# Optimization experiments

Hardware: AMD Instinct MI355X
Metric: run time of the kernel (lower is better)

The kernel has to match this reference:

```python
import jax, jax.numpy as jnp
import numpy as np

T, N, E = 12, 50000, 1_600_000
IN_DIM, H, H2, H3, AF, B = 12, 128, 256, 128, 10, 4096


def _sage(h, src, dst, Wl, Wr, b, n_nodes):
    # PyG SAGEConv (mean aggr): out = lin_l(mean_{j in N(i)} x_j) + lin_r(x_i)
    agg = jax.ops.segment_sum(h[src], dst, num_segments=n_nodes)
    deg = jax.ops.segment_sum(jnp.ones((src.shape[0],), h.dtype), dst, num_segments=n_nodes)
    mean = agg / jnp.clip(deg, 1.0)[:, None]
    return mean @ Wl.T + b + h @ Wr.T


def _attn(h, Wq, bq, Wk, bk, Wv, bv):
    # h: [N, T, H]; queries scaled by 1/sqrt(H) AFTER the linear (as in source)
    q = (h @ Wq.T + bq) / jnp.sqrt(jnp.asarray(h.shape[-1], h.dtype))
    k = h @ Wk.T + bk
    v = h @ Wv.T + bv
    w = jax.nn.softmax(jnp.einsum('nth,nsh->nts', q, k), axis=-1)
    return jnp.einsum('nts,nsh->nth', w, v)


def setup_inputs() -> dict:
    key = jax.random.key(0)
    ks = jax.random.split(key, 24)
    def lin(kw, out_d, in_d, scale=None):
        s = scale if scale is not None else 1.0 / np.sqrt(in_d)
        return jax.random.uniform(kw, (out_d, in_d), jnp.float32, -s, s)
    inp = {
        'x': jax.random.normal(ks[0], (T, N, IN_DIM), jnp.float32),
        'edge_index': jax.random.randint(ks[1], (2, E), 0, N, jnp.int64),
        'node_idx': jax.random.randint(ks[2], (B,), 0, N, jnp.int64),
        'apart_feature': jax.random.normal(ks[3], (B, AF), jnp.float32),
        'conv1_Wl': lin(ks[4], H, IN_DIM), 'conv1_Wr': lin(ks[5], H, IN_DIM),
        'conv1_b': jnp.zeros((H,), jnp.float32),
        'conv2_Wl': lin(ks[6], H, H), 'conv2_Wr': lin(ks[7], H, H),
        'conv2_b': jnp.zeros((H,), jnp.float32),
        'Wq': lin(ks[8], H, H), 'bq': jnp.zeros((H,), jnp.float32),
        'Wk': lin(ks[9], H, H), 'bk': jnp.zeros((H,), jnp.float32),
        'Wv': lin(ks[10], H, H), 'bv': jnp.zeros((H,), jnp.float32),
        'fc1_W': lin(ks[11], H2, H + AF), 'fc1_b': jnp.zeros((H2,), jnp.float32),
        'fc2_W': lin(ks[12], H3, H2), 'fc2_b': jnp.zeros((H3,), jnp.float32),
        'fc3_W': lin(ks[13], 1, H3), 'fc3_b': jnp.zeros((1,), jnp.float32),
    }
    return inp


def reference(x, edge_index, node_idx, apart_feature,
              conv1_Wl, conv1_Wr, conv1_b, conv2_Wl, conv2_Wr, conv2_b,
              Wq, bq, Wk, bk, Wv, bv,
              fc1_W, fc1_b, fc2_W, fc2_b, fc3_W, fc3_b):
    src, dst = edge_index[0], edge_index[1]
    n_nodes = x.shape[1]
    # conv1 per time slot (small fixed loop over T, matching the source)
    emb = jnp.stack([
        jax.nn.relu(_sage(x[i], src, dst, conv1_Wl, conv1_Wr, conv1_b, n_nodes))
        for i in range(x.shape[0])], axis=0)  # [T, N, H]
    emb = _attn(emb.transpose(1, 0, 2), Wq, bq, Wk, bk, Wv, bv).transpose(1, 0, 2)  # [T, N, H]
    emb = jnp.stack([
        jax.nn.relu(_sage(emb[i], src, dst, conv2_Wl, conv2_Wr, conv2_b, n_nodes))
        for i in range(emb.shape[0])], axis=0)  # [T, N, H]
    emb = _attn(emb.transpose(1, 0, 2), Wq, bq, Wk, bk, Wv, bv).sum(axis=1)  # [N, H]
    h = jnp.concatenate([emb[node_idx], apart_feature], axis=1)  # [B, H+AF]
    h = jax.nn.leaky_relu(h @ fc1_W.T + fc1_b, negative_slope=0.1)
    h = jax.nn.leaky_relu(h @ fc2_W.T + fc2_b, negative_slope=0.05)
    return h @ fc3_W.T + fc3_b  # [B, 1]
```

## Files before the change

### kernel.cpp

```cpp
#include <hip/hip_runtime.h>
#include <hip/hip_bf16.h>
#include <cstddef>
#include <cstdint>
#include <cmath>

typedef __attribute__((ext_vector_type(8))) short bf16x8v;
typedef __attribute__((ext_vector_type(4))) float f32x4;

__device__ inline unsigned short f2bf(float x) {
    uint32_t u = __float_as_uint(x);
    uint32_t r = (u + 0x7fffu + ((u >> 16) & 1u)) >> 16;
    return (unsigned short)r;
}

__device__ inline uint32_t pack2(float a, float b) {
    return (uint32_t)f2bf(a) | ((uint32_t)f2bf(b) << 16);
}

__device__ inline void unpack8(bf16x8v v, float* f) {
    union { bf16x8v v8; uint32_t u[4]; } cv; cv.v8 = v;
    #pragma unroll
    for (int d = 0; d < 4; d++) {
        uint32_t w = cv.u[d];
        f[2 * d]     = __uint_as_float(w << 16);
        f[2 * d + 1] = __uint_as_float(w & 0xffff0000u);
    }
}


__global__ __launch_bounds__(256) void prep0_kernel(
    const float* __restrict__ x, unsigned short* __restrict__ xTb, int N, int TB,
    const float* __restrict__ c2Wl, const float* __restrict__ c2Wr,
    const float* __restrict__ fc1W, const float* __restrict__ fc2W,
    const float* __restrict__ Wq, const float* __restrict__ Wk, const float* __restrict__ Wv,
    const float* __restrict__ c1Wl, const float* __restrict__ c1Wr,
    const float* __restrict__ bq,
    unsigned short* __restrict__ W2pack,
    float* __restrict__ fc1Wt, float* __restrict__ fc2Wt,
    unsigned short* __restrict__ Bpack, unsigned short* __restrict__ W1pack,
    unsigned short* __restrict__ Mpack, float* __restrict__ rvec,
    int* __restrict__ deg, int* __restrict__ cur) {
    __shared__ __align__(16) unsigned short sm[64][144];
    int b = blockIdx.x;
    int tid = threadIdx.x;
    if (b < TB) {
        int n0 = b * 64;
        int nodes = min(64, N - n0);
        for (int t = 0; t < 12; t++) {
            const float* src = x + ((size_t)t * N + n0) * 12;
            for (int k = tid; k < nodes * 12; k += 256)
                sm[k / 12][t * 12 + k % 12] = f2bf(src[k]);
        }
        __syncthreads();
        int chunks = nodes * 18;
        const uint4* smv = (const uint4*)&sm[0][0];
        uint4* dst = (uint4*)(xTb + (size_t)n0 * 144);
        for (int c = tid; c < chunks; c += 256) dst[c] = smv[c];
        return;
    }
    b -= TB;
    if (b < 667) {
        const float qscale = 0.08838834764831845f;
        int idx = b * 256 + tid;
        if (idx < 32768) {
            int i = idx & 7, l = (idx >> 3) & 63, nt = (idx >> 9) & 7, kc = idx >> 12;
            int col = nt * 16 + (l & 15);
            int k = kc * 32 + (l >> 4) * 8 + i;
            float v = (k < 128) ? c2Wl[col * 128 + k] : c2Wr[col * 128 + k - 128];
            W2pack[idx] = f2bf(v);
            return;
        }
        idx -= 32768;
        if (idx < 35328) { fc1Wt[(idx % 138) * 256 + idx / 138] = fc1W[idx]; return; }
        idx -= 35328;
        if (idx < 32768) { fc2Wt[(idx % 256) * 128 + idx / 256] = fc2W[idx]; return; }
        idx -= 32768;
        if (idx < 3 * 16384) {
            int p = idx >> 14, rem = idx & 16383;
            int kc = rem >> 12, rem2 = rem & 4095;
            int nt = rem2 >> 9, li = rem2 & 511;
            int l = li >> 3, i = li & 7;
            int col = nt * 16 + (l & 15);
            int j = kc * 32 + (l >> 4) * 8 + i;
            const float* W = (p == 0) ? Wq : (p == 1) ? Wk : Wv;
            Bpack[idx] = f2bf(W[col * 128 + j]);
            return;
        }
        idx -= 3 * 16384;
        if (idx < 4096) {
            int nt = idx >> 9, rem = idx & 511;
            int l = rem >> 3, i = rem & 7;
            int col = nt * 16 + (l & 15);
            int k = (l >> 4) * 8 + i;
            float v = (k < 12) ? c1Wl[col * 12 + k] : ((k < 24) ? c1Wr[col * 12 + k - 12] : 0.0f);
            W1pack[idx] = f2bf(v);
            return;
        }
        idx -= 4096;
        if (idx < 16384) {
            int kc = idx >> 12, rem2 = idx & 4095;
            int nt = rem2 >> 9, li = rem2 & 511;
            int l = li >> 3, i = li & 7;
            int col = nt * 16 + (l & 15);
            int j = kc * 32 + (l >> 4) * 8 + i;
            float sum = 0.f;
            for (int c = 0; c < 128; c++) sum += Wq[c * 128 + j] * Wk[c * 128 + col];
            Mpack[idx] = f2bf(qscale * sum);
            return;
        }
        idx -= 16384;
        if (idx < 128) {
            float sum = 0.f;
            for (int c = 0; c < 128; c++) sum += bq[c] * Wk[c * 128 + idx];
            rvec[idx] = qscale * sum;
        }
        return;
    }
    b -= 667;
    int idx = b * 256 + tid;
    if (idx < N) deg[idx] = 0;
    else if (idx < 2 * N) cur[idx - N] = 0;
}

__global__ void deg_kernel(const int* __restrict__ ei, int* __restrict__ deg, int E) {
    int e = blockIdx.x * 256 + threadIdx.x;
    if (e < E) atomicAdd(&deg[ei[E + e]], 1);
}

__global__ void scan_kernel(const int* __restrict__ deg, int* __restrict__ rs, int N) {
    __shared__ int part[1024];
    int tid = threadIdx.x;
    int chunk = (N + 1023) >> 10;
    int base = tid * chunk;
    int s = 0;
    for (int k = 0; k < chunk; k++) { int i = base + k; if (i < N) s += deg[i]; }
    part[tid] = s;
    __syncthreads();
    for (int off = 1; off < 1024; off <<= 1) {
        int v = (tid >= off) ? part[tid - off] : 0;
        __syncthreads();
        part[tid] += v;
        __syncthreads();
    }
    int run = part[tid] - s;
    for (int k = 0; k < chunk; k++) {
        int i = base + k;
        if (i < N) { rs[i] = run; run += deg[i]; }
    }
    if (tid == 1023) rs[N] = part[1023];
}

__global__ void fill_kernel(const int* __restrict__ ei, const int* __restrict__ rs,
                            int* __restrict__ cur, int* __restrict__ csr, int E) {
    int e = blockIdx.x * 256 + threadIdx.x;
    if (e < E) {
        int d = ei[E + e];
        int pos = atomicAdd(&cur[d], 1);
        csr[rs[d] + pos] = ei[e];
    }
}

__global__ void sentinel_kernel(float* out, int n) {
    int i = blockIdx.x * 256 + threadIdx.x;
    if (i < n) out[i] = 12345.0f;
}


__global__ __launch_bounds__(128) void fused1_kernel(
    const unsigned short* __restrict__ xTb, const int* __restrict__ rs,
    const int* __restrict__ csr, const unsigned short* __restrict__ W1pack,
    const float* __restrict__ b1, const unsigned short* __restrict__ Mpack,
    const float* __restrict__ rvec, const unsigned short* __restrict__ Vpack,
    const float* __restrict__ bv, unsigned short* __restrict__ emb1, int N) {
    __shared__ __align__(16) unsigned short lds[8448];
    int tid = threadIdx.x;
    int w = tid >> 6, l = tid & 63;
    int g = l >> 4, lam = l & 15;
    int node = blockIdx.x * 2 + w;
    if (node >= N) return;
    unsigned short* L = lds + w * 4224;
    unsigned short* s_cat = L;
    float* s_part = (float*)(L + 2176);
    const bf16x8v zero8 = (bf16x8v){0, 0, 0, 0, 0, 0, 0, 0};

    int beg = rs[node], end = rs[node + 1];
    int group = l / 18, d8 = l - group * 18;
    if (group < 3) {
        float acc[8] = {0.f, 0.f, 0.f, 0.f, 0.f, 0.f, 0.f, 0.f};
        int e = beg + group;
        for (; e + 21 < end; e += 24) {
            int nn[8];
            #pragma unroll
            for (int u = 0; u < 8; u++) nn[u] = csr[e + u * 3];
            bf16x8v vv[8];
            #pragma unroll
            for (int u = 0; u < 8; u++)
                vv[u] = *(const bf16x8v*)(xTb + (size_t)nn[u] * 144 + d8 * 8);
            #pragma unroll
            for (int u = 0; u < 8; u++) {
                float f[8]; unpack8(vv[u], f);
                #pragma unroll
                for (int i = 0; i < 8; i++) acc[i] += f[i];
            }
        }
        for (; e + 9 < end; e += 12) {
            int n0 = csr[e], n1 = csr[e + 3], n2 = csr[e + 6], n3 = csr[e + 9];
            bf16x8v v0 = *(const bf16x8v*)(xTb + (size_t)n0 * 144 + d8 * 8);
            bf16x8v v1 = *(const bf16x8v*)(xTb + (size_t)n1 * 144 + d8 * 8);
            bf16x8v v2 = *(const bf16x8v*)(xTb + (size_t)n2 * 144 + d8 * 8);
            bf16x8v v3 = *(const bf16x8v*)(xTb + (size_t)n3 * 144 + d8 * 8);
            float f0[8], f1[8], f2[8], f3[8];
            unpack8(v0, f0); unpack8(v1, f1); unpack8(v2, f2); unpack8(v3, f3);
            #pragma unroll
            for (int i = 0; i < 8; i++) acc[i] += (f0[i] + f1[i]) + (f2[i] + f3[i]);
        }
        for (; e < end; e += 3) {
            int nbr = csr[e];
            bf16x8v v = *(const bf16x8v*)(xTb + (size_t)nbr * 144 + d8 * 8);
            float f[8]; unpack8(v, f);
            #pragma unroll
            for (int i = 0; i < 8; i++) acc[i] += f[i];
        }
        #pragma unroll
        for (int i = 0; i < 8; i++) s_part[group * 144 + i * 18 + d8] = acc[i];
    }
    if (l < 16) *(uint4*)&s_cat[l * 40 + 24] = make_uint4(0u, 0u, 0u, 0u);
    if (l < 18) {
        float inv = 1.0f / fmaxf((float)(end - beg), 1.0f);
        bf16x8v sv = *(const bf16x8v*)(xTb + (size_t)node * 144 + l * 8);
        #pragma unroll
        for (int i = 0; i < 8; i++) {
            int d = l * 8 + i;
            int t = d / 12, f = d - t * 12;
            int j = i * 18 + l;
            float m = (s_part[j] + s_part[144 + j] + s_part[288 + j]) * inv;
            s_cat[t * 40 + f] = f2bf(m);
            s_cat[t * 40 + 12 + f] = ((unsigned short*)&sv)[i];
        }
    }

    bf16x8v a1 = (lam < 12) ? *(const bf16x8v*)&s_cat[lam * 40 + g * 8] : zero8;
    bf16x8v bfa[8];
    #pragma unroll
    for (int nt = 0; nt < 8; nt++) bfa[nt] = *(const bf16x8v*)(W1pack + nt * 512 + l * 8);
    f32x4 c1[8];
    #pragma unroll
    for (int nt = 0; nt < 8; nt++)
        c1[nt] = __builtin_amdgcn_mfma_f32_16x16x32_bf16(a1, bfa[nt], (f32x4){0.f, 0.f, 0.f, 0.f}, 0, 0, 0);
    #pragma unroll
    for (int nt = 0; nt < 8; nt++) {
        float bias = b1[nt * 16 + lam];
        #pragma unroll
        for (int r = 0; r < 4; r++)
            L[(4 * g + r) * 136 + nt * 16 + lam] = f2bf(fmaxf(c1[nt][r] + bias, 0.0f));
    }

    bf16x8v ha[4];
    #pragma unroll
    for (int kc = 0; kc < 4; kc++)
        ha[kc] = (lam < 12) ? *(const bf16x8v*)&L[lam * 136 + kc * 32 + g * 8] : zero8;

    f32x4 cg[8];
    #pragma unroll
    for (int nt = 0; nt < 8; nt++) cg[nt] = (f32x4){0.f, 0.f, 0.f, 0.f};
    #pragma unroll
    for (int kc = 0; kc < 4; kc++) {
        #pragma unroll
        for (int nt = 0; nt < 8; nt++)
            bfa[nt] = *(const bf16x8v*)(Mpack + (kc * 8 + nt) * 512 + l * 8);
        #pragma unroll
        for (int nt = 0; nt < 8; nt++)
            cg[nt] = __builtin_amdgcn_mfma_f32_16x16x32_bf16(ha[kc], bfa[nt], cg[nt], 0, 0, 0);
    }
    #pragma unroll
    for (int nt = 0; nt < 8; nt++) {
        float rv = rvec[nt * 16 + lam];
        #pragma unroll
        for (int r = 0; r < 4; r++)
            L[(4 * g + r) * 136 + nt * 16 + lam] = f2bf(cg[nt][r] + rv);
    }

    f32x4 cv[8];
    #pragma unroll
    for (int nt = 0; nt < 8; nt++) cv[nt] = (f32x4){0.f, 0.f, 0.f, 0.f};
    #pragma unroll
    for (int kc = 0; kc < 4; kc++) {
        #pragma unroll
        for (int nt = 0; nt < 8; nt++)
            bfa[nt] = *(const bf16x8v*)(Vpack + (kc * 8 + nt) * 512 + l * 8);
        #pragma unroll
        for (int nt = 0; nt < 8; nt++)
            cv[nt] = __builtin_amdgcn_mfma_f32_16x16x32_bf16(ha[kc], bfa[nt], cv[nt], 0, 0, 0);
    }
    #pragma unroll
    for (int nt = 0; nt < 8; nt++) {
        float bb = bv[nt * 16 + lam];
        uint32_t w0 = pack2(cv[nt][0] + bb, cv[nt][1] + bb);
        uint32_t w1 = pack2(cv[nt][2] + bb, cv[nt][3] + bb);
        *(uint2*)&L[2176 + (nt * 16 + lam) * 16 + 4 * g] = make_uint2(w0, w1);
    }

    f32x4 sc = (f32x4){0.f, 0.f, 0.f, 0.f};
    #pragma unroll
    for (int kc = 0; kc < 4; kc++) {
        bf16x8v ga = (lam < 12) ? *(const bf16x8v*)&L[lam * 136 + kc * 32 + g * 8] : zero8;
        sc = __builtin_amdgcn_mfma_f32_16x16x32_bf16(ga, ha[kc], sc, 0, 0, 0);
    }
    #pragma unroll
    for (int r = 0; r < 4; r++) {
        float s = (lam < 12) ? sc[r] : -3.0e38f;
        float mx = s;
        mx = fmaxf(mx, __shfl_xor(mx, 1)); mx = fmaxf(mx, __shfl_xor(mx, 2));
        mx = fmaxf(mx, __shfl_xor(mx, 4)); mx = fmaxf(mx, __shfl_xor(mx, 8));
        float e = __expf(s - mx);
        float sm = e;
        sm += __shfl_xor(sm, 1); sm += __shfl_xor(sm, 2);
        sm += __shfl_xor(sm, 4); sm += __shfl_xor(sm, 8);
        L[(4 * g + r) * 16 + lam] = f2bf(e / sm);
    }

    bf16x8v bw = (g < 2) ? *(const bf16x8v*)&L[lam * 16 + g * 8] : zero8;
    #pragma unroll
    for (int nt = 0; nt < 8; nt++) {
        bf16x8v av = (g < 2) ? *(const bf16x8v*)&L[2176 + (nt * 16 + lam) * 16 + g * 8] : zero8;
        f32x4 o = __builtin_amdgcn_mfma_f32_16x16x32_bf16(av, bw, (f32x4){0.f, 0.f, 0.f, 0.f}, 0, 0, 0);
        if (lam < 12) {
            uint32_t w0 = pack2(o[0], o[1]);
            uint32_t w1 = pack2(o[2], o[3]);
            *(uint2*)(emb1 + (size_t)node * 1536 + lam * 128 + nt * 16 + 4 * g) = make_uint2(w0, w1);
        }
    }
}


template <int SUM>
__global__ __launch_bounds__(64) void mfma_attn_kernel(
    unsigned short* io, const unsigned short* __restrict__ Bpack,
    const float* __restrict__ bq, const float* __restrict__ bk, const float* __restrict__ bv,
    float* __restrict__ outF, int totalRows) {
    __shared__ __align__(16) unsigned short lds[19712];
    int l = threadIdx.x;
    int g = l >> 4, lam = l & 15;
    int baseRow = blockIdx.x * 48;

    bf16x8v afrag[3][4];
    #pragma unroll
    for (int rt = 0; rt < 3; rt++) {
        int row = baseRow + rt * 16 + lam;
        if (row > totalRows - 1) row = totalRows - 1;
        #pragma unroll
        for (int kc = 0; kc < 4; kc++)
            afrag[rt][kc] = *(const bf16x8v*)(io + (size_t)row * 128 + kc * 32 + g * 8);
    }
    const float qscale = 0.08838834764831845f;

    #pragma unroll
    for (int p = 0; p < 3; p++) {
        f32x4 acc[3][8];
        #pragma unroll
        for (int rt = 0; rt < 3; rt++)
            #pragma unroll
            for (int nt = 0; nt < 8; nt++) acc[rt][nt] = (f32x4){0.f, 0.f, 0.f, 0.f};
        const unsigned short* Bp = Bpack + p * 16384;
        #pragma unroll
        for (int kc = 0; kc < 4; kc++) {
            #pragma unroll
            for (int nt = 0; nt < 8; nt++) {
                bf16x8v bfrag = *(const bf16x8v*)(Bp + (kc * 8 + nt) * 512 + l * 8);
                #pragma unroll
                for (int rt = 0; rt < 3; rt++)
                    acc[rt][nt] = __builtin_amdgcn_mfma_f32_16x16x32_bf16(afrag[rt][kc], bfrag, acc[rt][nt], 0, 0, 0);
            }
        }
        const float* bias = (p == 0) ? bq : (p == 1) ? bk : bv;
        #pragma unroll
        for (int nt = 0; nt < 8; nt++) {
            float bval = bias[nt * 16 + lam];
            #pragma unroll
            for (int rt = 0; rt < 3; rt++) {
                int row0 = 16 * rt + 4 * g;
                if (p < 2) {
                    int base = (p == 0) ? 0 : 6528;
                    #pragma unroll
                    for (int r = 0; r < 4; r++) {
                        float val = acc[rt][nt][r] + bval;
                        if (p == 0) val *= qscale;
                        lds[base + (row0 + r) * 136 + nt * 16 + lam] = f2bf(val);
                    }
                } else {
                    uint32_t w0 = pack2(acc[rt][nt][0] + bval, acc[rt][nt][1] + bval);
                    uint32_t w1 = pack2(acc[rt][nt][2] + bval, acc[rt][nt][3] + bval);
                    *(uint2*)&lds[13056 + (nt * 16 + lam) * 52 + row0] = make_uint2(w0, w1);
                }
            }
        }
    }
    __syncthreads();

    float wv[4][4];
    #pragma unroll
    for (int n = 0; n < 4; n++) {
        int qrow = 12 * n + lam;
        if (qrow > 47) qrow = 47;
        f32x4 sc = (f32x4){0.f, 0.f, 0.f, 0.f};
        #pragma unroll
        for (int kc = 0; kc < 4; kc++) {
            bf16x8v qa = *(const bf16x8v*)&lds[qrow * 136 + kc * 32 + g * 8];
            bf16x8v kb = *(const bf16x8v*)&lds[6528 + qrow * 136 + kc * 32 + g * 8];
            sc = __builtin_amdgcn_mfma_f32_16x16x32_bf16(qa, kb, sc, 0, 0, 0);
        }
        #pragma unroll
        for (int r = 0; r < 4; r++) {
            float s = (lam < 12) ? sc[r] : -3.0e38f;
            float mx = s;
            mx = fmaxf(mx, __shfl_xor(mx, 1)); mx = fmaxf(mx, __shfl_xor(mx, 2));
            mx = fmaxf(mx, __shfl_xor(mx, 4)); mx = fmaxf(mx, __shfl_xor(mx, 8));
            float e = __expf(s - mx);
            float sm = e;
            sm += __shfl_xor(sm, 1); sm += __shfl_xor(sm, 2);
            sm += __shfl_xor(sm, 4); sm += __shfl_xor(sm, 8);
            wv[n][r] = e / sm;
        }
    }
    __syncthreads();
    #pragma unroll
    for (int n = 0; n < 4; n++)
        #pragma unroll
        for (int r = 0; r < 4; r++)
            lds[(n * 16 + 4 * g + r) * 24 + lam] = f2bf(wv[n][r]);
    __syncthreads();

    const bf16x8v zero8 = (bf16x8v){0, 0, 0, 0, 0, 0, 0, 0};
    #pragma unroll
    for (int n = 0; n < 4; n++) {
        bf16x8v wfrag = zero8;
        if (g < 2) wfrag = *(const bf16x8v*)&lds[(n * 16 + lam) * 24 + g * 8];
        int sA = 12 * n + g * 8;
        int sB = sA + 4;
        if (sB > 44) sB = 44;
        #pragma unroll
        for (int nt = 0; nt < 8; nt++) {
            bf16x8v vfrag = zero8;
            if (g < 2) {
                int dbase = 13056 + (nt * 16 + lam) * 52;
                uint2 lo = *(const uint2*)&lds[dbase + sA];
                uint2 hi = *(const uint2*)&lds[dbase + sB];
                union { uint32_t u[4]; bf16x8v v; } cvv;
                cvv.u[0] = lo.x; cvv.u[1] = lo.y; cvv.u[2] = hi.x; cvv.u[3] = hi.y;
                vfrag = cvv.v;
            }
            f32x4 o = __builtin_amdgcn_mfma_f32_16x16x32_bf16(vfrag, wfrag, (f32x4){0.f, 0.f, 0.f, 0.f}, 0, 0, 0);
            if constexpr (SUM == 0) {
                if (lam < 12) {
                    int row = baseRow + 12 * n + lam;
                    if (row < totalRows) {
                        uint32_t w0 = pack2(o[0], o[1]);
                        uint32_t w1 = pack2(o[2], o[3]);
                        *(uint2*)(io + (size_t)row * 128 + nt * 16 + 4 * g) = make_uint2(w0, w1);
                    }
                }
            } else {
                #pragma unroll
                for (int r = 0; r < 4; r++) {
                    float v = (lam < 12) ? o[r] : 0.f;
                    v += __shfl_xor(v, 1); v += __shfl_xor(v, 2);
                    v += __shfl_xor(v, 4); v += __shfl_xor(v, 8);
                    o[r] = v;
                }
                if (lam == 0 && (baseRow + 12 * n) < totalRows) {
                    int node = blockIdx.x * 4 + n;
                    *(float4*)(outF + (size_t)node * 128 + nt * 16 + 4 * g) =
                        make_float4(o[0], o[1], o[2], o[3]);
                }
            }
        }
    }
}


__global__ __launch_bounds__(256) void conv2_kernel(
    const unsigned short* __restrict__ emb1, const int* __restrict__ node_idx,
    const int* __restrict__ rs, const int* __restrict__ csr,
    const unsigned short* __restrict__ W2pack, const float* __restrict__ b2,
    unsigned short* __restrict__ emb2) {
    int bb = blockIdx.x, tid = threadIdx.x;
    int n = node_idx[bb];
    __shared__ __align__(16) unsigned short s_cat[12][264];
    __shared__ __align__(16) unsigned short s_tile[12][128];
    int beg = rs[n], end = rs[n + 1];
    if (tid < 192) {
        float acc[8] = {0.f, 0.f, 0.f, 0.f, 0.f, 0.f, 0.f, 0.f};
        int e = beg;
        for (; e + 3 < end; e += 4) {
            int n0 = csr[e], n1 = csr[e + 1], n2 = csr[e + 2], n3 = csr[e + 3];
            bf16x8v v0 = *(const bf16x8v*)(emb1 + (size_t)n0 * 1536 + tid * 8);
            bf16x8v v1 = *(const bf16x8v*)(emb1 + (size_t)n1 * 1536 + tid * 8);
            bf16x8v v2 = *(const bf16x8v*)(emb1 + (size_t)n2 * 1536 + tid * 8);
            bf16x8v v3 = *(const bf16x8v*)(emb1 + (size_t)n3 * 1536 + tid * 8);
            float f0[8], f1[8], f2[8], f3[8];
            unpack8(v0, f0); unpack8(v1, f1); unpack8(v2, f2); unpack8(v3, f3);
            #pragma unroll
            for (int i = 0; i < 8; i++) acc[i] += (f0[i] + f1[i]) + (f2[i] + f3[i]);
        }
        for (; e < end; e++) {
            int nbr = csr[e];
            bf16x8v v = *(const bf16x8v*)(emb1 + (size_t)nbr * 1536 + tid * 8);
            float f[8]; unpack8(v, f);
            #pragma unroll
            for (int i = 0; i < 8; i++) acc[i] += f[i];
        }
        float inv = 1.0f / fmaxf((float)(end - beg), 1.0f);
        uint32_t w[4];
        #pragma unroll
        for (int d = 0; d < 4; d++)
            w[d] = pack2(acc[2 * d] * inv, acc[2 * d + 1] * inv);
        *(uint4*)&s_cat[tid >> 4][(tid & 15) * 8] = make_uint4(w[0], w[1], w[2], w[3]);
    } else {
        for (int c = tid - 192; c < 192; c += 64) {
            uint4 v = *(const uint4*)(emb1 + (size_t)n * 1536 + c * 8);
            *(uint4*)&s_cat[c >> 4][128 + (c & 15) * 8] = v;
        }
    }
    __syncthreads();
    if (tid < 64) {
        int g = tid >> 4, lam = tid & 15;
        const bf16x8v zero8 = (bf16x8v){0, 0, 0, 0, 0, 0, 0, 0};
        f32x4 acc2[8];
        #pragma unroll
        for (int nt = 0; nt < 8; nt++) acc2[nt] = (f32x4){0.f, 0.f, 0.f, 0.f};
        #pragma unroll
        for (int kc = 0; kc < 8; kc++) {
            bf16x8v a = (lam < 12) ? *(const bf16x8v*)&s_cat[lam][kc * 32 + g * 8] : zero8;
            #pragma unroll
            for (int nt = 0; nt < 8; nt++) {
                bf16x8v bf = *(const bf16x8v*)(W2pack + (kc * 8 + nt) * 512 + tid * 8);
                acc2[nt] = __builtin_amdgcn_mfma_f32_16x16x32_bf16(a, bf, acc2[nt], 0, 0, 0);
            }
        }
        if (g < 3) {
            #pragma unroll
            for (int nt = 0; nt < 8; nt++) {
                float bias = b2[nt * 16 + lam];
                #pragma unroll
                for (int r = 0; r < 4; r++)
                    s_tile[4 * g + r][nt * 16 + lam] = f2bf(fmaxf(acc2[nt][r] + bias, 0.0f));
            }
        }
    }
    __syncthreads();
    if (tid < 192)
        ((uint4*)(emb2 + (size_t)bb * 1536))[tid] = ((const uint4*)&s_tile[0][0])[tid];
}


__global__ __launch_bounds__(256) void head_kernel(
    const float* __restrict__ embF, const float* __restrict__ apart, const float* __restrict__ fc1Wt,
    const float* __restrict__ fc1b, const float* __restrict__ fc2Wt, const float* __restrict__ fc2b,
    const float* __restrict__ fc3W, const float* __restrict__ fc3b, float* __restrict__ out) {
    int bb = blockIdx.x, tid = threadIdx.x;
    __shared__ float in_s[138], a1[256], a2[128], red[128];
    if (tid < 128) in_s[tid] = embF[(size_t)bb * 128 + tid];
    else if (tid < 138) in_s[tid] = apart[(size_t)bb * 10 + tid - 128];
    __syncthreads();
    float o = fc1b[tid];
    for (int j = 0; j < 138; j++) o += in_s[j] * fc1Wt[j * 256 + tid];
    a1[tid] = o >= 0.f ? o : 0.1f * o;
    __syncthreads();
    if (tid < 128) {
        float o2 = fc2b[tid];
        for (int j = 0; j < 256; j++) o2 += a1[j] * fc2Wt[j * 128 + tid];
        a2[tid] = o2 >= 0.f ? o2 : 0.05f * o2;
    }
    __syncthreads();
    if (tid < 128) red[tid] = a2[tid] * fc3W[tid];
    __syncthreads();
    for (int s = 64; s > 0; s >>= 1) {
        if (tid < s) red[tid] += red[tid + s];
        __syncthreads();
    }
    if (tid == 0) out[bb] = red[0] + fc3b[0];
}


extern "C" void kernel_launch(void* const* d_in, const int* in_sizes, int n_in,
                              void* d_out, int out_size, void* d_ws, size_t ws_size,
                              hipStream_t stream) {
    const float* x    = (const float*)d_in[0];
    const int* ei     = (const int*)d_in[1];
    const int* nidx   = (const int*)d_in[2];
    const float* apart= (const float*)d_in[3];
    const float* c1Wl = (const float*)d_in[4];
    const float* c1Wr = (const float*)d_in[5];
    const float* c1b  = (const float*)d_in[6];
    const float* c2Wl = (const float*)d_in[7];
    const float* c2Wr = (const float*)d_in[8];
    const float* c2b  = (const float*)d_in[9];
    const float* Wq   = (const float*)d_in[10];
    const float* bq   = (const float*)d_in[11];
    const float* Wk   = (const float*)d_in[12];
    const float* bk   = (const float*)d_in[13];
    const float* Wv   = (const float*)d_in[14];
    const float* bv   = (const float*)d_in[15];
    const float* fc1W = (const float*)d_in[16];
    const float* fc1b = (const float*)d_in[17];
    const float* fc2W = (const float*)d_in[18];
    const float* fc2b = (const float*)d_in[19];
    const float* fc3W = (const float*)d_in[20];
    const float* fc3b = (const float*)d_in[21];

    int N = in_sizes[0] / 144;
    int E = in_sizes[1] / 2;
    int B = in_sizes[2];
    float* out = (float*)d_out;
    char* ws = (char*)d_ws;

    size_t off = 0;
    auto A = [&](size_t bytes) -> void* {
        void* q = ws + off;
        off = (off + bytes + 255) & ~(size_t)255;
        return q;
    };
    unsigned short* emb1 = (unsigned short*)A((size_t)N * 1536 * 2);
    size_t xtBytes = (size_t)N * 144 * 2;
    unsigned short* xTb = (unsigned short*)A(xtBytes);
    unsigned short* emb2;
    if ((size_t)B * 1536 * 2 <= xtBytes) emb2 = xTb;
    else emb2 = (unsigned short*)A((size_t)B * 1536 * 2);
    float* embF  = (float*)A((size_t)B * 128 * 4);
    unsigned short* Bpack  = (unsigned short*)A(3 * 16384 * 2);
    unsigned short* W1pack = (unsigned short*)A(4096 * 2);
    unsigned short* W2pack = (unsigned short*)A(32768 * 2);
    unsigned short* Mpack  = (unsigned short*)A(16384 * 2);
    float* rvec  = (float*)A(128 * 4);
    float* fc1Wt = (float*)A(138 * 256 * 4);
    float* fc2Wt = (float*)A(256 * 128 * 4);
    int* deg = (int*)A((size_t)N * 4);
    int* rsb = (int*)A((size_t)(N + 1) * 4);
    int* cur = (int*)A((size_t)N * 4);
    int* csr = (int*)A((size_t)E * 4);
    if (off > ws_size) {
        sentinel_kernel<<<(out_size + 255) / 256, 256, 0, stream>>>(out, out_size);
        return;
    }

    int TB = (N + 63) / 64;
    int ZB = (2 * N + 255) / 256;
    prep0_kernel<<<TB + 667 + ZB, 256, 0, stream>>>(
        x, xTb, N, TB,
        c2Wl, c2Wr, fc1W, fc2W, Wq, Wk, Wv, c1Wl, c1Wr, bq,
        W2pack, fc1Wt, fc2Wt, Bpack, W1pack, Mpack, rvec, deg, cur);

    int eb = (E + 255) / 256;
    deg_kernel<<<eb, 256, 0, stream>>>(ei, deg, E);
    scan_kernel<<<1, 1024, 0, stream>>>(deg, rsb, N);
    fill_kernel<<<eb, 256, 0, stream>>>(ei, rsb, cur, csr, E);

    fused1_kernel<<<(N + 1) / 2, 128, 0, stream>>>(
        xTb, rsb, csr, W1pack, c1b, Mpack, rvec, Bpack + 2 * 16384, bv, emb1, N);

    conv2_kernel<<<B, 256, 0, stream>>>(emb1, nidx, rsb, csr, W2pack, c2b, emb2);

    int rows2 = B * 12;
    mfma_attn_kernel<1><<<(rows2 + 47) / 48, 64, 0, stream>>>(emb2, Bpack, bq, bk, bv, embF, rows2);

    head_kernel<<<B, 256, 0, stream>>>(embF, apart, fc1Wt, fc1b, fc2Wt, fc2b, fc3W, fc3b, out);
}
```

Before: 653.3 us.

## Fuse conv2, second attention and MLP head into one per-node kernel

Replaces three kernels (conv2, second attention, head) with a single kernel per batch node. The neighbour gather is unrolled by 8 instead of 4, and the attention uses the precomputed Mpack/rvec folded Q·K form already used in fused1. This removes two launches and the emb2/embF global round trips. The cost is that only one wavefront does the MFMA work while the other three sit idle, and the longer kernel holds more registers and LDS.

Measured after the change: 673.2 us. 3.0% more time.

```diff
diff --git a/kernel.cpp b/kernel.cpp
--- a/kernel.cpp
+++ b/kernel.cpp
@@ -333,81 +333,138 @@
 }
 
 
-template <int SUM>
-__global__ __launch_bounds__(64) void mfma_attn_kernel(
-    unsigned short* io, const unsigned short* __restrict__ Bpack,
-    const float* __restrict__ bq, const float* __restrict__ bk, const float* __restrict__ bv,
-    float* __restrict__ outF, int totalRows) {
-    __shared__ __align__(16) unsigned short lds[19712];
-    int l = threadIdx.x;
-    int g = l >> 4, lam = l & 15;
-    int baseRow = blockIdx.x * 48;
-
-    bf16x8v afrag[3][4];
-    #pragma unroll
-    for (int rt = 0; rt < 3; rt++) {
-        int row = baseRow + rt * 16 + lam;
-        if (row > totalRows - 1) row = totalRows - 1;
+__global__ __launch_bounds__(256) void fused2_kernel(
+    const unsigned short* __restrict__ emb1, const int* __restrict__ node_idx,
+    const int* __restrict__ rs, const int* __restrict__ csr,
+    const unsigned short* __restrict__ W2pack, const float* __restrict__ b2,
+    const unsigned short* __restrict__ Mpack, const float* __restrict__ rvec,
+    const unsigned short* __restrict__ Vpack, const float* __restrict__ bv,
+    const float* __restrict__ apart,
+    const float* __restrict__ fc1Wt, const float* __restrict__ fc1b,
+    const float* __restrict__ fc2Wt, const float* __restrict__ fc2b,
+    const float* __restrict__ fc3W, const float* __restrict__ fc3b,
+    float* __restrict__ out) {
+    __shared__ __align__(16) unsigned short s_cat[12 * 264];
+    __shared__ __align__(16) unsigned short A[4224];
+    __shared__ float hd[128];
+    __shared__ float in_s[138], ah1[256], ah2[128];
+    int bb = blockIdx.x, tid = threadIdx.x;
+    int n = node_idx[bb];
+    int beg = rs[n], end = rs[n + 1];
+    const bf16x8v zero8 = (bf16x8v){0, 0, 0, 0, 0, 0, 0, 0};
+
+    if (tid < 192) {
+        float acc[8] = {0.f, 0.f, 0.f, 0.f, 0.f, 0.f, 0.f, 0.f};
+        int e = beg;
+        for (; e + 7 < end; e += 8) {
+            int nn[8];
+            #pragma unroll
+            for (int u = 0; u < 8; u++) nn[u] = csr[e + u];
+            bf16x8v vv[8];
+            #pragma unroll
+            for (int u = 0; u < 8; u++)
+                vv[u] = *(const bf16x8v*)(emb1 + (size_t)nn[u] * 1536 + tid * 8);
+            #pragma unroll
+            for (int u = 0; u < 8; u++) {
+                float f[8]; unpack8(vv[u], f);
+                #pragma unroll
+                for (int i = 0; i < 8; i++) acc[i] += f[i];
+            }
+        }
+        for (; e < end; e++) {
+            int nbr = csr[e];
+            bf16x8v v = *(const bf16x8v*)(emb1 + (size_t)nbr * 1536 + tid * 8);
+            float f[8]; unpack8(v, f);
+            #pragma unroll
+            for (int i = 0; i < 8; i++) acc[i] += f[i];
+        }
+        float inv = 1.0f / fmaxf((float)(end - beg), 1.0f);
+        uint32_t w[4];
+        #pragma unroll
+        for (int d = 0; d < 4; d++)
+            w[d] = pack2(acc[2 * d] * inv, acc[2 * d + 1] * inv);
+        *(uint4*)&s_cat[(tid >> 4) * 264 + (tid & 15) * 8] = make_uint4(w[0], w[1], w[2], w[3]);
+    } else {
+        for (int c = tid - 192; c < 192; c += 64) {
+            uint4 v = *(const uint4*)(emb1 + (size_t)n * 1536 + c * 8);
+            *(uint4*)&s_cat[(c >> 4) * 264 + 128 + (c & 15) * 8] = v;
+        }
+    }
+    __syncthreads();
+
+    if (tid < 64) {
+        int l = tid, g = l >> 4, lam = l & 15;
+        f32x4 acc2[8];
+        #pragma unroll
+        for (int nt = 0; nt < 8; nt++) acc2[nt] = (f32x4){0.f, 0.f, 0.f, 0.f};
+        #pragma unroll
+        for (int kc = 0; kc < 8; kc++) {
+            bf16x8v a = (lam < 12) ? *(const bf16x8v*)&s_cat[lam * 264 + kc * 32 + g * 8] : zero8;
+            #pragma unroll
+            for (int nt = 0; nt < 8; nt++) {
+                bf16x8v bf = *(const bf16x8v*)(W2pack + (kc * 8 + nt) * 512 + l * 8);
+                acc2[nt] = __builtin_amdgcn_mfma_f32_16x16x32_bf16(a, bf, acc2[nt], 0, 0, 0);
+            }
+        }
+        #pragma unroll
+        for (int nt = 0; nt < 8; nt++) {
+            float bias = b2[nt * 16 + lam];
+            #pragma unroll
+            for (int r = 0; r < 4; r++)
+                A[(4 * g + r) * 136 + nt * 16 + lam] = f2bf(fmaxf(acc2[nt][r] + bias, 0.0f));
+        }
+
+        bf16x8v ha[4];
         #pragma unroll
         for (int kc = 0; kc < 4; kc++)
-            afrag[rt][kc] = *(const bf16x8v*)(io + (size_t)row * 128 + kc * 32 + g * 8);
-    }
-    const float qscale = 0.08838834764831845f;
-
-    #pragma unroll
-    for (int p = 0; p < 3; p++) {
-        f32x4 acc[3][8];
-        #pragma unroll
-        for (int rt = 0; rt < 3; rt++)
-            #pragma unroll
-            for (int nt = 0; nt < 8; nt++) acc[rt][nt] = (f32x4){0.f, 0.f, 0.f, 0.f};
-        const unsigned short* Bp = Bpack + p * 16384;
+            ha[kc] = (lam < 12) ? *(const bf16x8v*)&A[lam * 136 + kc * 32 + g * 8] : zero8;
+
+        f32x4 cg[8];
+        bf16x8v bfa[8];
+        #pragma unroll
+        for (int nt = 0; nt < 8; nt++) cg[nt] = (f32x4){0.f, 0.f, 0.f, 0.f};
         #pragma unroll
         for (int kc = 0; kc < 4; kc++) {
             #pragma unroll
-            for (int nt = 0; nt < 8; nt++) {
-                bf16x8v bfrag = *(const bf16x8v*)(Bp + (kc * 8 + nt) * 512 + l * 8);
-                #pragma unroll
-                for (int rt = 0; rt < 3; rt++)
-                    acc[rt][nt] = __builtin_amdgcn_mfma_f32_16x16x32_bf16(afrag[rt][kc], bfrag, acc[rt][nt], 0, 0, 0);
-            }
-        }
-        const float* bias = (p == 0) ? bq : (p == 1) ? bk : bv;
+            for (int nt = 0; nt < 8; nt++)
+                bfa[nt] = *(const bf16x8v*)(Mpack + (kc * 8 + nt) * 512 + l * 8);
+            #pragma unroll
+            for (int nt = 0; nt < 8; nt++)
+                cg[nt] = __builtin_amdgcn_mfma_f32_16x16x32_bf16(ha[kc], bfa[nt], cg[nt], 0, 0, 0);
+        }
         #pragma unroll
         for (int nt = 0; nt < 8; nt++) {
-            float bval = bias[nt * 16 + lam];
-            #pragma unroll
-            for (int rt = 0; rt < 3; rt++) {
-                int row0 = 16 * rt + 4 * g;
-                if (p < 2) {
-                    int base = (p == 0) ? 0 : 6528;
-                    #pragma unroll
-                    for (int r = 0; r < 4; r++) {
-                        float val = acc[rt][nt][r] + bval;
-                        if (p == 0) val *= qscale;
-                        lds[base + (row0 + r) * 136 + nt * 16 + lam] = f2bf(val);
-                    }
-                } else {
-                    uint32_t w0 = pack2(acc[rt][nt][0] + bval, acc[rt][nt][1] + bval);
-                    uint32_t w1 = pack2(acc[rt][nt][2] + bval, acc[rt][nt][3] + bval);
-                    *(uint2*)&lds[13056 + (nt * 16 + lam) * 52 + row0] = make_uint2(w0, w1);
-                }
-            }
-        }
-    }
-    __syncthreads();
-
-    float wv[4][4];
-    #pragma unroll
-    for (int n = 0; n < 4; n++) {
-        int qrow = 12 * n + lam;
-        if (qrow > 47) qrow = 47;
+            float rv = rvec[nt * 16 + lam];
+            #pragma unroll
+            for (int r = 0; r < 4; r++)
+                A[(4 * g + r) * 136 + nt * 16 + lam] = f2bf(cg[nt][r] + rv);
+        }
+
+        f32x4 cvv[8];
+        #pragma unroll
+        for (int nt = 0; nt < 8; nt++) cvv[nt] = (f32x4){0.f, 0.f, 0.f, 0.f};
+        #pragma unroll
+        for (int kc = 0; kc < 4; kc++) {
+            #pragma unroll
+            for (int nt = 0; nt < 8; nt++)
+                bfa[nt] = *(const bf16x8v*)(Vpack + (kc * 8 + nt) * 512 + l * 8);
+            #pragma unroll
+            for (int nt = 0; nt < 8; nt++)
+                cvv[nt] = __builtin_amdgcn_mfma_f32_16x16x32_bf16(ha[kc], bfa[nt], cvv[nt], 0, 0, 0);
+        }
+        #pragma unroll
+        for (int nt = 0; nt < 8; nt++) {
+            float bb2 = bv[nt * 16 + lam];
+            uint32_t w0 = pack2(cvv[nt][0] + bb2, cvv[nt][1] + bb2);
+            uint32_t w1 = pack2(cvv[nt][2] + bb2, cvv[nt][3] + bb2);
+            *(uint2*)&A[2176 + (nt * 16 + lam) * 16 + 4 * g] = make_uint2(w0, w1);
+        }
+
         f32x4 sc = (f32x4){0.f, 0.f, 0.f, 0.f};
         #pragma unroll
         for (int kc = 0; kc < 4; kc++) {
-            bf16x8v qa = *(const bf16x8v*)&lds[qrow * 136 + kc * 32 + g * 8];
-            bf16x8v kb = *(const bf16x8v*)&lds[6528 + qrow * 136 + kc * 32 + g * 8];
-            sc = __builtin_amdgcn_mfma_f32_16x16x32_bf16(qa, kb, sc, 0, 0, 0);
+            bf16x8v ga = (lam < 12) ? *(const bf16x8v*)&A[lam * 136 + kc * 32 + g * 8] : zero8;
+            sc = __builtin_amdgcn_mfma_f32_16x16x32_bf16(ga, ha[kc], sc, 0, 0, 0);
         }
         #pragma unroll
         for (int r = 0; r < 4; r++) {
@@ -419,166 +476,48 @@
             float sm = e;
             sm += __shfl_xor(sm, 1); sm += __shfl_xor(sm, 2);
             sm += __shfl_xor(sm, 4); sm += __shfl_xor(sm, 8);
-            wv[n][r] = e / sm;
+            A[(4 * g + r) * 16 + lam] = f2bf(e / sm);
+        }
+
+        bf16x8v bw = (g < 2) ? *(const bf16x8v*)&A[lam * 16 + g * 8] : zero8;
+        #pragma unroll
+        for (int nt = 0; nt < 8; nt++) {
+            bf16x8v av = (g < 2) ? *(const bf16x8v*)&A[2176 + (nt * 16 + lam) * 16 + g * 8] : zero8;
+            f32x4 o = __builtin_amdgcn_mfma_f32_16x16x32_bf16(av, bw, (f32x4){0.f, 0.f, 0.f, 0.f}, 0, 0, 0);
+            #pragma unroll
+            for (int r = 0; r < 4; r++) {
+                float v = (lam < 12) ? o[r] : 0.f;
+                v += __shfl_xor(v, 1); v += __shfl_xor(v, 2);
+                v += __shfl_xor(v, 4); v += __shfl_xor(v, 8);
+                o[r] = v;
+            }
+            if (lam == 0) {
+                #pragma unroll
+                for (int r = 0; r < 4; r++) hd[nt * 16 + 4 * g + r] = o[r];
+            }
         }
     }
     __syncthreads();
-    #pragma unroll
-    for (int n = 0; n < 4; n++)
-        #pragma unroll
-        for (int r = 0; r < 4; r++)
-            lds[(n * 16 + 4 * g + r) * 24 + lam] = f2bf(wv[n][r]);
-    __syncthreads();
-
-    const bf16x8v zero8 = (bf16x8v){0, 0, 0, 0, 0, 0, 0, 0};
-    #pragma unroll
-    for (int n = 0; n < 4; n++) {
-        bf16x8v wfrag = zero8;
-        if (g < 2) wfrag = *(const bf16x8v*)&lds[(n * 16 + lam) * 24 + g * 8];
-        int sA = 12 * n + g * 8;
-        int sB = sA + 4;
-        if (sB > 44) sB = 44;
-        #pragma unroll
-        for (int nt = 0; nt < 8; nt++) {
-            bf16x8v vfrag = zero8;
-            if (g < 2) {
-                int dbase = 13056 + (nt * 16 + lam) * 52;
-                uint2 lo = *(const uint2*)&lds[dbase + sA];
-                uint2 hi = *(const uint2*)&lds[dbase + sB];
-                union { uint32_t u[4]; bf16x8v v; } cvv;
-                cvv.u[0] = lo.x; cvv.u[1] = lo.y; cvv.u[2] = hi.x; cvv.u[3] = hi.y;
-                vfrag = cvv.v;
-            }
-            f32x4 o = __builtin_amdgcn_mfma_f32_16x16x32_bf16(vfrag, wfrag, (f32x4){0.f, 0.f, 0.f, 0.f}, 0, 0, 0);
-            if constexpr (SUM == 0) {
-                if (lam < 12) {
-                    int row = baseRow + 12 * n + lam;
-                    if (row < totalRows) {
-                        uint32_t w0 = pack2(o[0], o[1]);
-                        uint32_t w1 = pack2(o[2], o[3]);
-                        *(uint2*)(io + (size_t)row * 128 + nt * 16 + 4 * g) = make_uint2(w0, w1);
-                    }
-                }
-            } else {
-                #pragma unroll
-                for (int r = 0; r < 4; r++) {
-                    float v = (lam < 12) ? o[r] : 0.f;
-                    v += __shfl_xor(v, 1); v += __shfl_xor(v, 2);
-                    v += __shfl_xor(v, 4); v += __shfl_xor(v, 8);
-                    o[r] = v;
-                }
-                if (lam == 0 && (baseRow + 12 * n) < totalRows) {
-                    int node = blockIdx.x * 4 + n;
-                    *(float4*)(outF + (size_t)node * 128 + nt * 16 + 4 * g) =
-                        make_float4(o[0], o[1], o[2], o[3]);
-                }
-            }
-        }
-    }
-}
-
-
-__global__ __launch_bounds__(256) void conv2_kernel(
-    const unsigned short* __restrict__ emb1, const int* __restrict__ node_idx,
-    const int* __restrict__ rs, const int* __restrict__ csr,
-    const unsigned short* __restrict__ W2pack, const float* __restrict__ b2,
-    unsigned short* __restrict__ emb2) {
-    int bb = blockIdx.x, tid = threadIdx.x;
-    int n = node_idx[bb];
-    __shared__ __align__(16) unsigned short s_cat[12][264];
-    __shared__ __align__(16) unsigned short s_tile[12][128];
-    int beg = rs[n], end = rs[n + 1];
-    if (tid < 192) {
-        float acc[8] = {0.f, 0.f, 0.f, 0.f, 0.f, 0.f, 0.f, 0.f};
-        int e = beg;
-        for (; e + 3 < end; e += 4) {
-            int n0 = csr[e], n1 = csr[e + 1], n2 = csr[e + 2], n3 = csr[e + 3];
-            bf16x8v v0 = *(const bf16x8v*)(emb1 + (size_t)n0 * 1536 + tid * 8);
-            bf16x8v v1 = *(const bf16x8v*)(emb1 + (size_t)n1 * 1536 + tid * 8);
-            bf16x8v v2 = *(const bf16x8v*)(emb1 + (size_t)n2 * 1536 + tid * 8);
-            bf16x8v v3 = *(const bf16x8v*)(emb1 + (size_t)n3 * 1536 + tid * 8);
-            float f0[8], f1[8], f2[8], f3[8];
-            unpack8(v0, f0); unpack8(v1, f1); unpack8(v2, f2); unpack8(v3, f3);
-            #pragma unroll
-            for (int i = 0; i < 8; i++) acc[i] += (f0[i] + f1[i]) + (f2[i] + f3[i]);
-        }
-        for (; e < end; e++) {
-            int nbr = csr[e];
-            bf16x8v v = *(const bf16x8v*)(emb1 + (size_t)nbr * 1536 + tid * 8);
-            float f[8]; unpack8(v, f);
-            #pragma unroll
-            for (int i = 0; i < 8; i++) acc[i] += f[i];
-        }
-        float inv = 1.0f / fmaxf((float)(end - beg), 1.0f);
-        uint32_t w[4];
-        #pragma unroll
-        for (int d = 0; d < 4; d++)
-            w[d] = pack2(acc[2 * d] * inv, acc[2 * d + 1] * inv);
-        *(uint4*)&s_cat[tid >> 4][(tid & 15) * 8] = make_uint4(w[0], w[1], w[2], w[3]);
-    } else {
-        for (int c = tid - 192; c < 192; c += 64) {
-            uint4 v = *(const uint4*)(emb1 + (size_t)n * 1536 + c * 8);
-            *(uint4*)&s_cat[c >> 4][128 + (c & 15) * 8] = v;
-        }
-    }
-    __syncthreads();
-    if (tid < 64) {
-        int g = tid >> 4, lam = tid & 15;
-        const bf16x8v zero8 = (bf16x8v){0, 0, 0, 0, 0, 0, 0, 0};
-        f32x4 acc2[8];
-        #pragma unroll
-        for (int nt = 0; nt < 8; nt++) acc2[nt] = (f32x4){0.f, 0.f, 0.f, 0.f};
-        #pragma unroll
-        for (int kc = 0; kc < 8; kc++) {
-            bf16x8v a = (lam < 12) ? *(const bf16x8v*)&s_cat[lam][kc * 32 + g * 8] : zero8;
-            #pragma unroll
-            for (int nt = 0; nt < 8; nt++) {
-                bf16x8v bf = *(const bf16x8v*)(W2pack + (kc * 8 + nt) * 512 + tid * 8);
-                acc2[nt] = __builtin_amdgcn_mfma_f32_16x16x32_bf16(a, bf, acc2[nt], 0, 0, 0);
-            }
-        }
-        if (g < 3) {
-            #pragma unroll
-            for (int nt = 0; nt < 8; nt++) {
-                float bias = b2[nt * 16 + lam];
-                #pragma unroll
-                for (int r = 0; r < 4; r++)
-                    s_tile[4 * g + r][nt * 16 + lam] = f2bf(fmaxf(acc2[nt][r] + bias, 0.0f));
-            }
-        }
-    }
-    __syncthreads();
-    if (tid < 192)
-        ((uint4*)(emb2 + (size_t)bb * 1536))[tid] = ((const uint4*)&s_tile[0][0])[tid];
-}
-
-
-__global__ __launch_bounds__(256) void head_kernel(
-    const float* __restrict__ embF, const float* __restrict__ apart, const float* __restrict__ fc1Wt,
-    const float* __restrict__ fc1b, const float* __restrict__ fc2Wt, const float* __restrict__ fc2b,
-    const float* __restrict__ fc3W, const float* __restrict__ fc3b, float* __restrict__ out) {
-    int bb = blockIdx.x, tid = threadIdx.x;
-    __shared__ float in_s[138], a1[256], a2[128], red[128];
-    if (tid < 128) in_s[tid] = embF[(size_t)bb * 128 + tid];
+
+    if (tid < 128) in_s[tid] = hd[tid];
     else if (tid < 138) in_s[tid] = apart[(size_t)bb * 10 + tid - 128];
     __syncthreads();
     float o = fc1b[tid];
     for (int j = 0; j < 138; j++) o += in_s[j] * fc1Wt[j * 256 + tid];
-    a1[tid] = o >= 0.f ? o : 0.1f * o;
+    ah1[tid] = o >= 0.f ? o : 0.1f * o;
     __syncthreads();
     if (tid < 128) {
         float o2 = fc2b[tid];
-        for (int j = 0; j < 256; j++) o2 += a1[j] * fc2Wt[j * 128 + tid];
-        a2[tid] = o2 >= 0.f ? o2 : 0.05f * o2;
-    }
-    __syncthreads();
-    if (tid < 128) red[tid] = a2[tid] * fc3W[tid];
+        for (int j = 0; j < 256; j++) o2 += ah1[j] * fc2Wt[j * 128 + tid];
+        float a2 = o2 >= 0.f ? o2 : 0.05f * o2;
+        ah2[tid] = a2 * fc3W[tid];
+    }
     __syncthreads();
     for (int s = 64; s > 0; s >>= 1) {
-        if (tid < s) red[tid] += red[tid + s];
+        if (tid < s) ah2[tid] += ah2[tid + s];
         __syncthreads();
     }
-    if (tid == 0) out[bb] = red[0] + fc3b[0];
+    if (tid == 0) out[bb] = ah2[0] + fc3b[0];
 }
 
 
@@ -621,12 +560,7 @@
         return q;
     };
     unsigned short* emb1 = (unsigned short*)A((size_t)N * 1536 * 2);
-    size_t xtBytes = (size_t)N * 144 * 2;
-    unsigned short* xTb = (unsigned short*)A(xtBytes);
-    unsigned short* emb2;
-    if ((size_t)B * 1536 * 2 <= xtBytes) emb2 = xTb;
-    else emb2 = (unsigned short*)A((size_t)B * 1536 * 2);
-    float* embF  = (float*)A((size_t)B * 128 * 4);
+    unsigned short* xTb = (unsigned short*)A((size_t)N * 144 * 2);
     unsigned short* Bpack  = (unsigned short*)A(3 * 16384 * 2);
     unsigned short* W1pack = (unsigned short*)A(4096 * 2);
     unsigned short* W2pack = (unsigned short*)A(32768 * 2);
@@ -658,10 +592,7 @@
     fused1_kernel<<<(N + 1) / 2, 128, 0, stream>>>(
         xTb, rsb, csr, W1pack, c1b, Mpack, rvec, Bpack + 2 * 16384, bv, emb1, N);
 
-    conv2_kernel<<<B, 256, 0, stream>>>(emb1, nidx, rsb, csr, W2pack, c2b, emb2);
-
-    int rows2 = B * 12;
-    mfma_attn_kernel<1><<<(rows2 + 47) / 48, 64, 0, stream>>>(emb2, Bpack, bq, bk, bv, embF, rows2);
-
-    head_kernel<<<B, 256, 0, stream>>>(embF, apart, fc1Wt, fc1b, fc2Wt, fc2b, fc3W, fc3b, out);
-}
+    fused2_kernel<<<B, 256, 0, stream>>>(
+        emb1, nidx, rsb, csr, W2pack, c2b, Mpack, rvec, Bpack + 2 * 16384, bv,
+        apart, fc1Wt, fc1b, fc2Wt, fc2b, fc3W, fc3b, out);
+}
```
